# Performance work log

Hardware: AMD Instinct MI355X
Metric: run time of the kernel (lower is better)

## Reference

```python
import jax, jax.numpy as jnp
import numpy as np

N, n, m, k = 100000, 32, 16, 32
MU = 100.0  # bubble kernel scale (init arg mu)


def setup_inputs() -> dict:
    key = jax.random.key(0)
    ks = jax.random.split(key, 7)
    x = jax.random.normal(ks[0], (N,), dtype=jnp.float32)
    # torch.nn.Linear(N, n): weight [n, N], bias [n]
    encoder_w = jax.random.normal(ks[1], (n, N), dtype=jnp.float32) / np.float32(np.sqrt(N))
    encoder_b = jnp.zeros((n,), dtype=jnp.float32)
    # decoder parameter [n, N]
    decoder = jax.random.normal(ks[2], (n, N), dtype=jnp.float32) / np.float32(np.sqrt(n))
    # torch.nn.Linear(n, n*m): weight [n*m, n], bias [n*m]
    bw_w = jax.random.normal(ks[3], (n * m, n), dtype=jnp.float32) / np.float32(np.sqrt(n))
    bw_b = jnp.zeros((n * m,), dtype=jnp.float32)
    neighbour_distance = jax.random.uniform(ks[4], (N, k), dtype=jnp.float32)
    neighbour_id = jax.random.randint(ks[5], (N, k), 0, N)
    clustering_labels = jax.random.randint(ks[6], (N,), 0, m)
    return {
        "x": x,
        "encoder_w": encoder_w,
        "encoder_b": encoder_b,
        "decoder": decoder,
        "bw_w": bw_w,
        "bw_b": bw_b,
        "neighbour_distance": neighbour_distance,
        "neighbour_id": neighbour_id,
        "clustering_labels": clustering_labels,
    }


def reference(x, encoder_w, encoder_b, decoder, bw_w, bw_b,
              neighbour_distance, neighbour_id, clustering_labels):
    # encode: [N] -> [n]
    encoded = x @ encoder_w.T + encoder_b
    # per-basis, per-cluster bandwidths: sigmoid(Linear)/60 -> [n, m] -> expand to [n, N]
    bandwidths = jax.nn.sigmoid(encoded @ bw_w.T + bw_b) / 60.0
    w = bandwidths.reshape(n, m)[:, clustering_labels]  # [n, N]
    # bubble window: relu(1 - d^2 / (w*mu)^2) -> [n, N, k]
    window = jax.nn.relu(1.0 - neighbour_distance[None, :, :] ** 2
                         / (w[:, :, None] * MU) ** 2)
    # normalization over axis 1 (the N axis), faithful to the source's dim=1
    window = window / jnp.sum(window, axis=1, keepdims=True)
    # gather decoder rows at neighbours, weight, reduce over k: [n, N]
    convolved_basis = jnp.sum(decoder[:, neighbour_id] * window, axis=-1)
    # [n] @ [n, N] -> [N]
    return encoded @ convolved_basis
```

## Files before the change

kernel.cpp:

```cpp
#include <hip/hip_runtime.h>
#include <hip/hip_fp16.h>

#define N_PTS 100000
#define MU_F  100.0f

typedef unsigned int uint;
typedef _Float16 h2 __attribute__((ext_vector_type(2)));
typedef float f2 __attribute__((ext_vector_type(2)));

#define E_SCALE 16384.0f
#define E_SCALE_INV (1.0f / 16384.0f)

static __device__ inline h2 h2pack(float a, float b) {
    return __builtin_bit_cast(h2, __builtin_amdgcn_cvt_pkrtz(a, b));
}
static __device__ inline float fdot2f(h2 a, h2 b, float c) {
    return __builtin_amdgcn_fdot2(a, b, c, false);
}
static __device__ inline h2 h2fma(h2 a, h2 b, h2 c) {
#if __has_builtin(__builtin_elementwise_fma)
    return __builtin_elementwise_fma(a, b, c);
#else
    return a * b + c;
#endif
}
static __device__ inline h2 h2max(h2 a, h2 b) {
#if __has_builtin(__builtin_elementwise_max)
    return __builtin_elementwise_max(a, b);
#else
    h2 r;
    r.x = a.x > b.x ? a.x : b.x;
    r.y = a.y > b.y ? a.y : b.y;
    return r;
#endif
}

#define ENC_BLKS 256
#define TR_BLKS  1563
#define S_BLKS   1024
#define S_PCH    98
#define NCOPY    8
#define NPAIRS   (N_PTS / 2)
#define M_BLKS   2048
#define M_CH     ((NPAIRS + M_BLKS - 1) / M_BLKS)


__global__ __launch_bounds__(256) void k_prep_tr(const float* __restrict__ x,
                                                 const float* __restrict__ encW,
                                                 const float* __restrict__ encB,
                                                 float* __restrict__ enc,
                                                 const float* __restrict__ dec,
                                                 __half* __restrict__ decT) {
    int b = blockIdx.x;
    if (b < ENC_BLKS) {
        int row = b & 31;
        int chunk = b >> 5;
        const int CH = N_PTS / 8;
        int base = chunk * CH;
        const float4* W4 = reinterpret_cast<const float4*>(encW + (size_t)row * N_PTS + base);
        const float4* x4 = reinterpret_cast<const float4*>(x + base);
        const int nv = CH / 4;
        float acc = 0.f;
        for (int idx = threadIdx.x; idx < nv; idx += 256) {
            float4 w = W4[idx];
            float4 xv = x4[idx];
            acc += w.x * xv.x + w.y * xv.y + w.z * xv.z + w.w * xv.w;
        }
        #pragma unroll
        for (int off = 32; off > 0; off >>= 1) acc += __shfl_down(acc, off);
        __shared__ float sred[4];
        int wid = threadIdx.x >> 6;
        if ((threadIdx.x & 63) == 0) sred[wid] = acc;
        __syncthreads();
        if (threadIdx.x == 0) {
            float s = sred[0] + sred[1] + sred[2] + sred[3];
            if (chunk == 0) s += encB[row];
            atomicAdd(enc + row, s);
        }
    } else {
        __shared__ float tile[32][65];
        int j0 = (b - ENC_BLKS) * 64;
        int col = threadIdx.x & 63;
        int r0 = threadIdx.x >> 6;
        #pragma unroll
        for (int it = 0; it < 8; ++it) {
            int row = it * 4 + r0;
            int j = j0 + col;
            float v = (j < N_PTS) ? dec[(size_t)row * N_PTS + j] : 0.f;
            tile[row][col] = v;
        }
        __syncthreads();
        #pragma unroll
        for (int it = 0; it < 4; ++it) {
            int idx = it * 256 + threadIdx.x;
            int j = idx >> 4;
            int p = idx & 15;
            int jj = j0 + j;
            if (jj < N_PTS) {
                __half2 h = __halves2half2(__float2half(tile[2 * p][j]),
                                           __float2half(tile[2 * p + 1][j]));
                *reinterpret_cast<__half2*>(decT + (size_t)jj * 32 + 2 * p) = h;
            }
        }
    }
}

__global__ __launch_bounds__(256) void k_tab(const float* __restrict__ enc_g,
                                             const float* __restrict__ bw_w,
                                             const float* __restrict__ bw_b,
                                             float* __restrict__ invFG,
                                             h2* __restrict__ invHLG) {
    __shared__ float encL[32];
    __shared__ float invF[512];
    if (threadIdx.x < 32) encL[threadIdx.x] = enc_g[threadIdx.x];
    __syncthreads();
    for (int r = threadIdx.x; r < 512; r += 256) {
        int i = r >> 4, c = r & 15;
        const float4* wr4 = reinterpret_cast<const float4*>(bw_w + (size_t)r * 32);
        float z = bw_b[r];
        #pragma unroll
        for (int p4 = 0; p4 < 8; ++p4) {
            float4 wv = wr4[p4];
            z = fmaf(encL[4 * p4 + 0], wv.x, z);
            z = fmaf(encL[4 * p4 + 1], wv.y, z);
            z = fmaf(encL[4 * p4 + 2], wv.z, z);
            z = fmaf(encL[4 * p4 + 3], wv.w, z);
        }
        float s = 1.f / (1.f + __expf(-z));
        float wmu = s * (MU_F / 60.0f);
        float iv = 1.f / (wmu * wmu);
        invF[c * 32 + i] = iv;
        invFG[c * 32 + i] = iv;
    }
    __syncthreads();
    {
        int t = threadIdx.x;
        int c = t >> 4, q = (t >> 2) & 3, tt = t & 3;
        int i0 = q * 8 + 2 * tt;
        invHLG[t] = h2pack(fminf(invF[c * 32 + i0], 6.0e4f),
                           fminf(invF[c * 32 + i0 + 1], 6.0e4f));
    }
}

__global__ __launch_bounds__(256, 8) void k_S(const float* __restrict__ invFG,
                                              const float* __restrict__ nd,
                                              const int* __restrict__ labels,
                                              float* __restrict__ S8) {
    __shared__ float invF[512];
    if (threadIdx.x < 128)
        reinterpret_cast<float4*>(invF)[threadIdx.x] =
            reinterpret_cast<const float4*>(invFG)[threadIdx.x];
    __syncthreads();

    int kk = threadIdx.x & 31;
    int ig = threadIdx.x >> 5;
    int start = blockIdx.x * S_PCH;
    int jend = min(start + S_PCH, N_PTS);

    float a0 = 0.f, a1 = 0.f, a2 = 0.f, a3 = 0.f;

    auto ld4 = [&](int jbase, float* d, int* cc) {
        #pragma unroll
        for (int u = 0; u < 4; ++u) {
            int j = jbase + u;
            int jc = min(j, N_PTS - 1);
            float dv = __builtin_nontemporal_load(&nd[(size_t)jc * 32 + kk]);
            cc[u] = labels[jc];
            d[u] = (j < jend) ? dv : 1.0e15f;
        }
    };
    float dA[4], dB[4], dC[4]; int cA[4], cB[4], cC[4];
    ld4(start, dA, cA);
    ld4(start + 4, dB, cB);
    for (int jj = start; jj < jend; jj += 4) {
        ld4(jj + 8, dC, cC);
        #pragma unroll
        for (int u = 0; u < 4; ++u) {
            float4 iv = *reinterpret_cast<const float4*>(&invF[cA[u] * 32 + ig * 4]);
            float d2 = dA[u] * dA[u];
            a0 += fmaxf(fmaf(d2, -iv.x, 1.f), 0.f);
            a1 += fmaxf(fmaf(d2, -iv.y, 1.f), 0.f);
            a2 += fmaxf(fmaf(d2, -iv.z, 1.f), 0.f);
            a3 += fmaxf(fmaf(d2, -iv.w, 1.f), 0.f);
        }
        #pragma unroll
        for (int u = 0; u < 4; ++u) {
            dA[u] = dB[u]; cA[u] = cB[u];
            dB[u] = dC[u]; cB[u] = cC[u];
        }
    }

    float* Sc = S8 + (size_t)(blockIdx.x & (NCOPY - 1)) * 1024;
    int cell = (ig * 4) * 32 + kk;
    atomicAdd(&Sc[cell], a0);
    atomicAdd(&Sc[cell + 32], a1);
    atomicAdd(&Sc[cell + 64], a2);
    atomicAdd(&Sc[cell + 96], a3);
}

__global__ __launch_bounds__(256, 6) void k_main(const h2* __restrict__ invHLG,
                                                 const float* __restrict__ enc_g,
                                                 const float* __restrict__ S8,
                                                 const float* __restrict__ nd,
                                                 const int* __restrict__ nid,
                                                 const int* __restrict__ labels,
                                                 const __half* __restrict__ decT,
                                                 float* __restrict__ out) {
    __shared__ h2 invHL[256];
    __shared__ float Sred[1024];
    if (threadIdx.x < 64)
        reinterpret_cast<uint4*>(invHL)[threadIdx.x] =
            reinterpret_cast<const uint4*>(invHLG)[threadIdx.x];
    for (int t = threadIdx.x; t < 1024; t += 256) {
        float s = 0.f;
        #pragma unroll
        for (int c = 0; c < NCOPY; ++c)
            s += S8[(size_t)c * 1024 + t];
        Sred[t] = s;
    }
    __syncthreads();

    int lane = threadIdx.x & 63;
    int R = lane >> 2;
    int q = lane & 3;

    h2 EhA[4], EhB[4];
    #pragma unroll
    for (int t = 0; t < 4; ++t) {
        int i0 = q * 8 + 2 * t;
        float e0 = enc_g[i0], e1 = enc_g[i0 + 1];
        float sA0 = Sred[i0 * 32 + R],      sA1 = Sred[(i0 + 1) * 32 + R];
        float sB0 = Sred[i0 * 32 + R + 16], sB1 = Sred[(i0 + 1) * 32 + R + 16];
        EhA[t] = h2pack(e0 / sA0 * E_SCALE, e1 / sA1 * E_SCALE);
        EhB[t] = h2pack(e0 / sB0 * E_SCALE, e1 / sB1 * E_SCALE);
    }
    const h2 zero2 = h2pack(0.f, 0.f);
    const h2 one2 = h2pack(1.f, 1.f);

    int w = threadIdx.x >> 6;
    int start = blockIdx.x * M_CH;
    int pend = min(start + M_CH, NPAIRS);
    int pa = start + w;
    const uint4* decQ = reinterpret_cast<const uint4*>(decT);
    if (pa >= pend) return;

    auto load_ldd = [&](int pc, int* id, float* dd, int& c0, int& c1) {
        pc = min(pc, NPAIRS - 1);
        int j0 = 2 * pc, j1 = j0 + 1;
        #pragma unroll
        for (int s = 0; s < 4; ++s) {
            size_t idx = (size_t)((s >> 1) ? j1 : j0) * 32 + (s & 1) * 16 + R;
            id[s] = __builtin_nontemporal_load(&nid[idx]);
            dd[s] = __builtin_nontemporal_load(&nd[idx]);
        }
        c0 = labels[j0];
        c1 = labels[j1];
    };
    auto load_rows = [&](const int* id, uint4* r) {
        #pragma unroll
        for (int s = 0; s < 4; ++s)
            r[s] = decQ[(size_t)id[s] * 4 + q];
    };
    auto load_ih = [&](int c0, int c1, h2* ih0, h2* ih1) {
        uint4 a = *reinterpret_cast<const uint4*>(&invHL[c0 * 16 + q * 4]);
        uint4 bq = *reinterpret_cast<const uint4*>(&invHL[c1 * 16 + q * 4]);
        ih0[0] = __builtin_bit_cast(h2, a.x);  ih0[1] = __builtin_bit_cast(h2, a.y);
        ih0[2] = __builtin_bit_cast(h2, a.z);  ih0[3] = __builtin_bit_cast(h2, a.w);
        ih1[0] = __builtin_bit_cast(h2, bq.x); ih1[1] = __builtin_bit_cast(h2, bq.y);
        ih1[2] = __builtin_bit_cast(h2, bq.z); ih1[3] = __builtin_bit_cast(h2, bq.w);
    };

    int ida[4], idb[4]; float dda[4], ddb[4];
    int ca0, ca1, cb0, cb1;
    uint4 ra[4], rb[4];
    h2 ihA0[4], ihA1[4];

    load_ldd(pa, ida, dda, ca0, ca1);
    load_ldd(pa + 4, idb, ddb, cb0, cb1);
    load_rows(ida, ra);
    load_ih(ca0, ca1, ihA0, ihA1);

    while (pa < pend) {
        load_rows(idb, rb);
        h2 ihB0[4], ihB1[4];
        load_ih(cb0, cb1, ihB0, ihB1);
        int idc[4]; float ddc[4]; int cc0, cc1;
        load_ldd(pa + 8, idc, ddc, cc0, cc1);

        float d20 = dda[0] * dda[0];
        float d21 = dda[1] * dda[1];
        float d22 = dda[2] * dda[2];
        float d23 = dda[3] * dda[3];
        h2 md0 = h2pack(-d20, -d20);
        h2 md1 = h2pack(-d21, -d21);
        h2 md2 = h2pack(-d22, -d22);
        h2 md3 = h2pack(-d23, -d23);

        float a0 = 0.f, a1 = 0.f, a2 = 0.f, a3 = 0.f;
        #pragma unroll
        for (int t = 0; t < 4; ++t) {
            uint dw0 = (t == 0) ? ra[0].x : (t == 1) ? ra[0].y : (t == 2) ? ra[0].z : ra[0].w;
            uint dw1 = (t == 0) ? ra[1].x : (t == 1) ? ra[1].y : (t == 2) ? ra[1].z : ra[1].w;
            uint dw2 = (t == 0) ? ra[2].x : (t == 1) ? ra[2].y : (t == 2) ? ra[2].z : ra[2].w;
            uint dw3 = (t == 0) ? ra[3].x : (t == 1) ? ra[3].y : (t == 2) ? ra[3].z : ra[3].w;
            {
                h2 wv = h2max(h2fma(md0, ihA0[t], one2), zero2);
                a0 = fdot2f(wv * EhA[t], __builtin_bit_cast(h2, dw0), a0);
            }
            {
                h2 wv = h2max(h2fma(md1, ihA0[t], one2), zero2);
                a1 = fdot2f(wv * EhB[t], __builtin_bit_cast(h2, dw1), a1);
            }
            {
                h2 wv = h2max(h2fma(md2, ihA1[t], one2), zero2);
                a2 = fdot2f(wv * EhA[t], __builtin_bit_cast(h2, dw2), a2);
            }
            {
                h2 wv = h2max(h2fma(md3, ihA1[t], one2), zero2);
                a3 = fdot2f(wv * EhB[t], __builtin_bit_cast(h2, dw3), a3);
            }
        }
        float u = a0 + a1;
        float v = a2 + a3;
        #pragma unroll
        for (int off = 32; off > 0; off >>= 1) {
            u += __shfl_xor(u, off);
            v += __shfl_xor(v, off);
        }
        if (lane == 0)  out[2 * pa]     = u * E_SCALE_INV;
        if (lane == 32) out[2 * pa + 1] = v * E_SCALE_INV;

        ca0 = cb0; ca1 = cb1; cb0 = cc0; cb1 = cc1;
        #pragma unroll
        for (int s = 0; s < 4; ++s) {
            dda[s] = ddb[s]; ddb[s] = ddc[s];
            ida[s] = idb[s]; idb[s] = idc[s];
            ra[s] = rb[s];
            ihA0[s] = ihB0[s]; ihA1[s] = ihB1[s];
        }
        pa += 4;
    }
}

extern "C" void kernel_launch(void* const* d_in, const int* in_sizes, int n_in,
                              void* d_out, int out_size, void* d_ws, size_t ws_size,
                              hipStream_t stream) {
    const float* x     = (const float*)d_in[0];
    const float* enc_w = (const float*)d_in[1];
    const float* enc_b = (const float*)d_in[2];
    const float* dec   = (const float*)d_in[3];
    const float* bw_w  = (const float*)d_in[4];
    const float* bw_b  = (const float*)d_in[5];
    const float* nd    = (const float*)d_in[6];
    const int*   nid   = (const int*)d_in[7];
    const int*   labels= (const int*)d_in[8];
    float* out = (float*)d_out;

    char* ws = (char*)d_ws;
    float* enc    = (float*)(ws + 0);
    float* S8     = (float*)(ws + 128);
    float* invFG  = (float*)(ws + 32896);
    h2*    invHLG = (h2*)(ws + 34944);
    __half* decT  = (__half*)(ws + 532480);

    (void)hipMemsetAsync(d_ws, 0, 32896, stream);
    k_prep_tr<<<dim3(ENC_BLKS + TR_BLKS), dim3(256), 0, stream>>>(
        x, enc_w, enc_b, enc, dec, decT);
    k_tab<<<dim3(1), dim3(256), 0, stream>>>(enc, bw_w, bw_b, invFG, invHLG);
    k_S<<<dim3(S_BLKS), dim3(256), 0, stream>>>(invFG, nd, labels, S8);
    k_main<<<dim3(M_BLKS), dim3(256), 0, stream>>>(invHLG, enc, S8, nd, nid,
                                                   labels, decT, out);
}
```

Baseline: 173.3 us.

## Split decoder gather into two half-basis passes over separate fp16 tables

```diff
diff --git a/kernel.cpp b/kernel.cpp
--- a/kernel.cpp
+++ b/kernel.cpp
@@ -40,9 +40,8 @@
 #define S_BLKS   1024
 #define S_PCH    98
 #define NCOPY    8
-#define NPAIRS   (N_PTS / 2)
 #define M_BLKS   2048
-#define M_CH     ((NPAIRS + M_BLKS - 1) / M_BLKS)
+#define M_PCH    49
 
 
 __global__ __launch_bounds__(256) void k_prep_tr(const float* __restrict__ x,
@@ -50,7 +49,8 @@
                                                  const float* __restrict__ encB,
                                                  float* __restrict__ enc,
                                                  const float* __restrict__ dec,
-                                                 __half* __restrict__ decT) {
+                                                 __half* __restrict__ decL,
+                                                 __half* __restrict__ decH) {
     int b = blockIdx.x;
     if (b < ENC_BLKS) {
         int row = b & 31;
@@ -99,7 +99,9 @@
             if (jj < N_PTS) {
                 __half2 h = __halves2half2(__float2half(tile[2 * p][j]),
                                            __float2half(tile[2 * p + 1][j]));
-                *reinterpret_cast<__half2*>(decT + (size_t)jj * 32 + 2 * p) = h;
+                __half* dst = (p < 8) ? (decL + (size_t)jj * 16 + 2 * p)
+                                      : (decH + (size_t)jj * 16 + 2 * (p - 8));
+                *reinterpret_cast<__half2*>(dst) = h;
             }
         }
     }
@@ -198,147 +200,96 @@
     atomicAdd(&Sc[cell + 96], a3);
 }
 
-__global__ __launch_bounds__(256, 6) void k_main(const h2* __restrict__ invHLG,
-                                                 const float* __restrict__ enc_g,
-                                                 const float* __restrict__ S8,
-                                                 const float* __restrict__ nd,
-                                                 const int* __restrict__ nid,
-                                                 const int* __restrict__ labels,
-                                                 const __half* __restrict__ decT,
-                                                 float* __restrict__ out) {
+__global__ __launch_bounds__(256) void k_elf(const float* __restrict__ enc_g,
+                                             const float* __restrict__ S8,
+                                             h2* __restrict__ EhG2) {
+    __shared__ float encL[32];
+    __shared__ float ELf[1024];
+    if (threadIdx.x < 32) encL[threadIdx.x] = enc_g[threadIdx.x];
+    __syncthreads();
+    for (int t = threadIdx.x; t < 1024; t += 256) {
+        float s = 0.f;
+        #pragma unroll
+        for (int c = 0; c < NCOPY; ++c)
+            s += S8[(size_t)c * 1024 + t];
+        ELf[t] = encL[t >> 5] / s * E_SCALE;
+    }
+    __syncthreads();
+    for (int e = threadIdx.x; e < 512; e += 256) {
+        int h = e >> 8, rem = e & 255;
+        int kk = rem >> 3, q = (rem >> 2) & 1, tt = rem & 3;
+        int i0 = h * 16 + q * 8 + 2 * tt;
+        EhG2[e] = h2pack(ELf[i0 * 32 + kk], ELf[(i0 + 1) * 32 + kk]);
+    }
+}
+
+__global__ __launch_bounds__(256, 8) void k_main_half(const h2* __restrict__ invHLG,
+                                                      const h2* __restrict__ EhG2h,
+                                                      const float* __restrict__ nd,
+                                                      const int* __restrict__ nid,
+                                                      const int* __restrict__ labels,
+                                                      const __half* __restrict__ decHlf,
+                                                      float* __restrict__ out,
+                                                      int h) {
     __shared__ h2 invHL[256];
-    __shared__ float Sred[1024];
     if (threadIdx.x < 64)
         reinterpret_cast<uint4*>(invHL)[threadIdx.x] =
             reinterpret_cast<const uint4*>(invHLG)[threadIdx.x];
-    for (int t = threadIdx.x; t < 1024; t += 256) {
-        float s = 0.f;
-        #pragma unroll
-        for (int c = 0; c < NCOPY; ++c)
-            s += S8[(size_t)c * 1024 + t];
-        Sred[t] = s;
-    }
     __syncthreads();
 
     int lane = threadIdx.x & 63;
-    int R = lane >> 2;
-    int q = lane & 3;
-
-    h2 EhA[4], EhB[4];
-    #pragma unroll
-    for (int t = 0; t < 4; ++t) {
-        int i0 = q * 8 + 2 * t;
-        float e0 = enc_g[i0], e1 = enc_g[i0 + 1];
-        float sA0 = Sred[i0 * 32 + R],      sA1 = Sred[(i0 + 1) * 32 + R];
-        float sB0 = Sred[i0 * 32 + R + 16], sB1 = Sred[(i0 + 1) * 32 + R + 16];
-        EhA[t] = h2pack(e0 / sA0 * E_SCALE, e1 / sA1 * E_SCALE);
-        EhB[t] = h2pack(e0 / sB0 * E_SCALE, e1 / sB1 * E_SCALE);
+    int kk = lane >> 1;
+    int q = lane & 1;
+
+    h2 Eh[4];
+    {
+        uint4 ev = reinterpret_cast<const uint4*>(EhG2h)[kk * 2 + q];
+        Eh[0] = __builtin_bit_cast(h2, ev.x); Eh[1] = __builtin_bit_cast(h2, ev.y);
+        Eh[2] = __builtin_bit_cast(h2, ev.z); Eh[3] = __builtin_bit_cast(h2, ev.w);
     }
     const h2 zero2 = h2pack(0.f, 0.f);
     const h2 one2 = h2pack(1.f, 1.f);
+    int ihOff = (h * 2 + q) * 4;
 
     int w = threadIdx.x >> 6;
-    int start = blockIdx.x * M_CH;
-    int pend = min(start + M_CH, NPAIRS);
-    int pa = start + w;
-    const uint4* decQ = reinterpret_cast<const uint4*>(decT);
-    if (pa >= pend) return;
-
-    auto load_ldd = [&](int pc, int* id, float* dd, int& c0, int& c1) {
-        pc = min(pc, NPAIRS - 1);
-        int j0 = 2 * pc, j1 = j0 + 1;
-        #pragma unroll
-        for (int s = 0; s < 4; ++s) {
-            size_t idx = (size_t)((s >> 1) ? j1 : j0) * 32 + (s & 1) * 16 + R;
-            id[s] = __builtin_nontemporal_load(&nid[idx]);
-            dd[s] = __builtin_nontemporal_load(&nd[idx]);
-        }
-        c0 = labels[j0];
-        c1 = labels[j1];
-    };
-    auto load_rows = [&](const int* id, uint4* r) {
-        #pragma unroll
-        for (int s = 0; s < 4; ++s)
-            r[s] = decQ[(size_t)id[s] * 4 + q];
-    };
-    auto load_ih = [&](int c0, int c1, h2* ih0, h2* ih1) {
-        uint4 a = *reinterpret_cast<const uint4*>(&invHL[c0 * 16 + q * 4]);
-        uint4 bq = *reinterpret_cast<const uint4*>(&invHL[c1 * 16 + q * 4]);
-        ih0[0] = __builtin_bit_cast(h2, a.x);  ih0[1] = __builtin_bit_cast(h2, a.y);
-        ih0[2] = __builtin_bit_cast(h2, a.z);  ih0[3] = __builtin_bit_cast(h2, a.w);
-        ih1[0] = __builtin_bit_cast(h2, bq.x); ih1[1] = __builtin_bit_cast(h2, bq.y);
-        ih1[2] = __builtin_bit_cast(h2, bq.z); ih1[3] = __builtin_bit_cast(h2, bq.w);
-    };
-
-    int ida[4], idb[4]; float dda[4], ddb[4];
-    int ca0, ca1, cb0, cb1;
-    uint4 ra[4], rb[4];
-    h2 ihA0[4], ihA1[4];
-
-    load_ldd(pa, ida, dda, ca0, ca1);
-    load_ldd(pa + 4, idb, ddb, cb0, cb1);
-    load_rows(ida, ra);
-    load_ih(ca0, ca1, ihA0, ihA1);
-
-    while (pa < pend) {
-        load_rows(idb, rb);
-        h2 ihB0[4], ihB1[4];
-        load_ih(cb0, cb1, ihB0, ihB1);
-        int idc[4]; float ddc[4]; int cc0, cc1;
-        load_ldd(pa + 8, idc, ddc, cc0, cc1);
-
-        float d20 = dda[0] * dda[0];
-        float d21 = dda[1] * dda[1];
-        float d22 = dda[2] * dda[2];
-        float d23 = dda[3] * dda[3];
-        h2 md0 = h2pack(-d20, -d20);
-        h2 md1 = h2pack(-d21, -d21);
-        h2 md2 = h2pack(-d22, -d22);
-        h2 md3 = h2pack(-d23, -d23);
-
-        float a0 = 0.f, a1 = 0.f, a2 = 0.f, a3 = 0.f;
-        #pragma unroll
-        for (int t = 0; t < 4; ++t) {
-            uint dw0 = (t == 0) ? ra[0].x : (t == 1) ? ra[0].y : (t == 2) ? ra[0].z : ra[0].w;
-            uint dw1 = (t == 0) ? ra[1].x : (t == 1) ? ra[1].y : (t == 2) ? ra[1].z : ra[1].w;
-            uint dw2 = (t == 0) ? ra[2].x : (t == 1) ? ra[2].y : (t == 2) ? ra[2].z : ra[2].w;
-            uint dw3 = (t == 0) ? ra[3].x : (t == 1) ? ra[3].y : (t == 2) ? ra[3].z : ra[3].w;
-            {
-                h2 wv = h2max(h2fma(md0, ihA0[t], one2), zero2);
-                a0 = fdot2f(wv * EhA[t], __builtin_bit_cast(h2, dw0), a0);
-            }
-            {
-                h2 wv = h2max(h2fma(md1, ihA0[t], one2), zero2);
-                a1 = fdot2f(wv * EhB[t], __builtin_bit_cast(h2, dw1), a1);
-            }
-            {
-                h2 wv = h2max(h2fma(md2, ihA1[t], one2), zero2);
-                a2 = fdot2f(wv * EhA[t], __builtin_bit_cast(h2, dw2), a2);
-            }
-            {
-                h2 wv = h2max(h2fma(md3, ihA1[t], one2), zero2);
-                a3 = fdot2f(wv * EhB[t], __builtin_bit_cast(h2, dw3), a3);
-            }
-        }
-        float u = a0 + a1;
-        float v = a2 + a3;
-        #pragma unroll
-        for (int off = 32; off > 0; off >>= 1) {
-            u += __shfl_xor(u, off);
-            v += __shfl_xor(v, off);
-        }
-        if (lane == 0)  out[2 * pa]     = u * E_SCALE_INV;
-        if (lane == 32) out[2 * pa + 1] = v * E_SCALE_INV;
-
-        ca0 = cb0; ca1 = cb1; cb0 = cc0; cb1 = cc1;
-        #pragma unroll
-        for (int s = 0; s < 4; ++s) {
-            dda[s] = ddb[s]; ddb[s] = ddc[s];
-            ida[s] = idb[s]; idb[s] = idc[s];
-            ra[s] = rb[s];
-            ihA0[s] = ihB0[s]; ihA1[s] = ihB1[s];
-        }
-        pa += 4;
+    int j0 = blockIdx.x * M_PCH;
+    int jend = min(j0 + M_PCH, N_PTS);
+    const uint4* decQ = reinterpret_cast<const uint4*>(decHlf);
+
+    for (int j = j0 + w; j < jend; j += 4) {
+        int c = labels[j];
+        size_t idx = (size_t)j * 32 + kk;
+        int id = __builtin_nontemporal_load(&nid[idx]);
+        float d = __builtin_nontemporal_load(&nd[idx]);
+        uint4 row = decQ[(size_t)id * 2 + q];
+        uint4 iv = *reinterpret_cast<const uint4*>(&invHL[c * 16 + ihOff]);
+
+        float d2 = d * d;
+        h2 md = h2pack(-d2, -d2);
+        float a = 0.f;
+        {
+            h2 wv = h2max(h2fma(md, __builtin_bit_cast(h2, iv.x), one2), zero2);
+            a = fdot2f(wv * Eh[0], __builtin_bit_cast(h2, row.x), a);
+        }
+        {
+            h2 wv = h2max(h2fma(md, __builtin_bit_cast(h2, iv.y), one2), zero2);
+            a = fdot2f(wv * Eh[1], __builtin_bit_cast(h2, row.y), a);
+        }
+        {
+            h2 wv = h2max(h2fma(md, __builtin_bit_cast(h2, iv.z), one2), zero2);
+            a = fdot2f(wv * Eh[2], __builtin_bit_cast(h2, row.z), a);
+        }
+        {
+            h2 wv = h2max(h2fma(md, __builtin_bit_cast(h2, iv.w), one2), zero2);
+            a = fdot2f(wv * Eh[3], __builtin_bit_cast(h2, row.w), a);
+        }
+        #pragma unroll
+        for (int off = 32; off > 0; off >>= 1) a += __shfl_xor(a, off);
+        if (lane == 0) {
+            float val = a * E_SCALE_INV;
+            if (h == 0) out[j] = val;
+            else        atomicAdd(&out[j], val);
+        }
     }
 }
 
@@ -361,13 +312,18 @@
     float* S8     = (float*)(ws + 128);
     float* invFG  = (float*)(ws + 32896);
     h2*    invHLG = (h2*)(ws + 34944);
-    __half* decT  = (__half*)(ws + 532480);
+    h2*    EhG2   = (h2*)(ws + 35968);
+    __half* decL  = (__half*)(ws + 532480);
+    __half* decH  = (__half*)(ws + 3732480);
 
     (void)hipMemsetAsync(d_ws, 0, 32896, stream);
     k_prep_tr<<<dim3(ENC_BLKS + TR_BLKS), dim3(256), 0, stream>>>(
-        x, enc_w, enc_b, enc, dec, decT);
+        x, enc_w, enc_b, enc, dec, decL, decH);
     k_tab<<<dim3(1), dim3(256), 0, stream>>>(enc, bw_w, bw_b, invFG, invHLG);
     k_S<<<dim3(S_BLKS), dim3(256), 0, stream>>>(invFG, nd, labels, S8);
-    k_main<<<dim3(M_BLKS), dim3(256), 0, stream>>>(invHLG, enc, S8, nd, nid,
-                                                   labels, decT, out);
-}
+    k_elf<<<dim3(1), dim3(256), 0, stream>>>(enc, S8, EhG2);
+    k_main_half<<<dim3(M_BLKS), dim3(256), 0, stream>>>(
+        invHLG, EhG2, nd, nid, labels, decL, out, 0);
+    k_main_half<<<dim3(M_BLKS), dim3(256), 0, stream>>>(
+        invHLG, EhG2 + 256, nd, nid, labels, decH, out, 1);
+}
```

After: 189.8 us. 9.5% more time.
